# Performance work log

Hardware: AMD Instinct MI355X
Metric: run time of the kernel (lower is better)

## Reference

```python
import jax, jax.numpy as jnp
import numpy as np

B = 4096
D = 512
N_IMG = 8


def setup_inputs() -> dict:
    key = jax.random.key(0)
    k1, k2 = jax.random.split(key)
    feat_query = jax.random.normal(k1, (B, D), dtype=jnp.float32)
    feat_gallery = jax.random.normal(k2, (B, D), dtype=jnp.float32)
    return {"feat_query": feat_query, "feat_gallery": feat_gallery, "batch_size_image": N_IMG}


def _forward(feat_query, feat_gallery, batch_size_image):
    b = feat_query.shape[0]
    labels = jnp.arange(b) // batch_size_image
    pos_full = (labels[:, None] == labels[None, :]).astype(feat_query.dtype)  # [B,B] block-diag
    neg_mask = 1.0 - pos_full
    pos_dist_diag = pos_full * 1e25
    pos_mask = pos_full - jnp.eye(b, dtype=feat_query.dtype)  # positives excluding self

    # squared euclidean pairwise distance: ||q||^2 + ||g||^2 - 2 q.g
    nq = jnp.sum(feat_query * feat_query, axis=1, keepdims=True)          # [B,1]
    ng = jnp.sum(feat_gallery * feat_gallery, axis=1, keepdims=True)      # [B,1]
    r = feat_query @ feat_gallery.T                                        # [B,B] GEMM
    distance = jnp.clip(nq + ng.T - 2.0 * r, 1e-8, None)

    dist_pos = distance * pos_mask
    dist_neg = distance * neg_mask + pos_dist_diag

    # --- sampling on stop-gradient copies (mirrors .data usage in torch) ---
    dp = jax.lax.stop_gradient(dist_pos)
    dn = jax.lax.stop_gradient(dist_neg)
    skey = jax.random.key(42)
    kp, kn = jax.random.split(skey)

    # multinomial over positive distances == categorical with zero-weight elsewhere
    neg_inf = jnp.float32(-jnp.inf)
    logw_pos = jnp.where(dp > 0, jnp.log(dp), neg_inf)
    pos_ids = jax.random.categorical(kp, logw_pos, axis=-1)                # [B]
    pscore = jnp.take_along_axis(dp, pos_ids[:, None], axis=1)[:, 0]       # [B]

    # uniform among negatives with dist < pscore + 1e-4; fallback to argmin
    hard_mask = dn < (pscore[:, None] + 1e-4)                              # [B,B]
    logw_neg = jnp.where(hard_mask, 0.0, neg_inf)
    neg_sampled = jax.random.categorical(kn, logw_neg, axis=-1)            # [B]
    neg_ids = jnp.where(hard_mask.any(axis=-1), neg_sampled, jnp.argmin(dn, axis=-1))

    score_pos = jnp.sqrt(jnp.take_along_axis(dist_pos, pos_ids[:, None], axis=1))  # [B,1]
    score_neg = jnp.sqrt(jnp.take_along_axis(dist_neg, neg_ids[:, None], axis=1))  # [B,1]

    # margin == 0 branch: softplus loss
    diff = 1e-4 + score_pos - score_neg
    loss = jnp.mean(jax.nn.softplus(diff))
    return loss


def reference(feat_query, feat_gallery, batch_size_image):
    return _forward(feat_query, feat_gallery, batch_size_image)
```

## Files before the change

kernel.cpp:

```cpp
#include <hip/hip_runtime.h>
#include <hip/hip_fp16.h>
#include <stdint.h>
#include <math.h>

#define B 4096
#define D 512
#define NIMG_SHIFT 3

#define BM 128
#define BN 128
#define NKS 8
#define NCH (B / BN)

typedef _Float16 f16x8 __attribute__((ext_vector_type(8)));
typedef float f32x4 __attribute__((ext_vector_type(4)));

#define LDSPTR(p) ((__attribute__((address_space(3))) void*)(p))
#define GLPTR(p)  ((const __attribute__((address_space(1))) void*)(p))

__device__ __half   Q2h[(size_t)B * D];
__device__ __half   G2h[(size_t)B * D];
__device__ float    nqd[B], ngd[B], psd[B], spd[B];
__device__ uint32_t bKeyd[NCH * B];
__device__ float    bDnd[NCH * B];
__device__ float    mDnd[NCH * B];
__device__ float    partd[B / 8];

__host__ __device__ inline void tf2x32(uint32_t k0, uint32_t k1,
                                       uint32_t x0, uint32_t x1,
                                       uint32_t& y0, uint32_t& y1) {
  const uint32_t ks2 = k0 ^ k1 ^ 0x1BD11BDAu;
  uint32_t v0 = x0 + k0, v1 = x1 + k1;
#define RR(r) { v0 += v1; v1 = (v1 << (r)) | (v1 >> (32 - (r))); v1 ^= v0; }
  RR(13) RR(15) RR(26) RR(6)   v0 += k1;  v1 += ks2 + 1u;
  RR(17) RR(29) RR(16) RR(24)  v0 += ks2; v1 += k0 + 2u;
  RR(13) RR(15) RR(26) RR(6)   v0 += k0;  v1 += k1 + 3u;
  RR(17) RR(29) RR(16) RR(24)  v0 += k1;  v1 += ks2 + 4u;
  RR(13) RR(15) RR(26) RR(6)   v0 += ks2; v1 += k0 + 5u;
#undef RR
  y0 = v0; y1 = v1;
}

__device__ inline uint32_t draw_bits(uint32_t key0, uint32_t key1, uint32_t flat) {
  uint32_t y0, y1;
  tf2x32(key0, key1, 0u, flat, y0, y1);
  return y1;
}

__device__ inline float gumbel_from_bits(uint32_t bits) {
  float f = __uint_as_float((bits >> 9) | 0x3f800000u) - 1.0f;
  float u = (f == 0.0f) ? 1.17549435e-38f : f;
  return -logf(-logf(u));
}

__global__ __launch_bounds__(256) void cvtn_k(const float* __restrict__ Q,
                                              const float* __restrict__ G) {
  int gtid = blockIdx.x * 256 + threadIdx.x;
  int wave = gtid >> 6;
  int lane = gtid & 63;
  if (wave >= 2 * B) return;
  const int isG = wave >= B;
  const float* src = isG ? G : Q;
  __half* dst = isG ? G2h : Q2h;
  const int row = isG ? wave - B : wave;
  const float4* p = (const float4*)(src + (size_t)row * D);
  float ssq = 0.0f;
#pragma unroll
  for (int i = 0; i < 2; i++) {
    const int e = lane + 64 * i;
    float4 v = p[e];
    const float* pv = (const float*)&v;
    __half hh[4] __attribute__((aligned(8)));
#pragma unroll
    for (int j = 0; j < 4; j++) {
      const float x = pv[j];
      ssq += x * x;
      hh[j] = __float2half(x);
    }
    *(uint2*)(dst + (size_t)row * D + e * 4) = *(const uint2*)hh;
  }
#pragma unroll
  for (int off = 32; off; off >>= 1) ssq += __shfl_xor(ssq, off, 64);
  if (lane == 0) { if (isG) ngd[row] = ssq; else nqd[row] = ssq; }
}

__global__ __launch_bounds__(256) void pos_k(const float* __restrict__ Q,
                                             const float* __restrict__ G,
                                             uint32_t kp0, uint32_t kp1) {
  __shared__ float Qs[8][D];
  __shared__ float Gs[8][D];
  __shared__ float dots[8][8];
  int t = threadIdx.x;
  int rbase = blockIdx.x * 8;
#pragma unroll
  for (int s = 0; s < 4; s++) {
    int idx = t + 256 * s;
    int rr = idx >> 7;
    int kk = idx & 127;
    ((float4*)&Qs[rr][0])[kk] = ((const float4*)(Q + (size_t)(rbase + rr) * D))[kk];
    ((float4*)&Gs[rr][0])[kk] = ((const float4*)(G + (size_t)(rbase + rr) * D))[kk];
  }
  __syncthreads();
  {
    int p = t >> 2;
    int part = t & 3;
    int i = p >> 3, j = p & 7;
    float s = 0.0f;
    int k0 = part * 128;
    for (int k = k0; k < k0 + 128; k++) s += Qs[i][k] * Gs[j][k];
    s += __shfl_xor(s, 1, 64);
    s += __shfl_xor(s, 2, 64);
    if (part == 0) dots[i][j] = s;
  }
  __syncthreads();
  if (t < 8) {
    int i = t;
    int r = rbase + i;
    float nqr = nqd[r];
    float best = -INFINITY;
    float bdp = 0.0f;
#pragma unroll
    for (int j = 0; j < 8; j++) {
      if (j == i) continue;
      int c = rbase + j;
      float dp = fmaxf(nqr + ngd[c] - 2.0f * dots[i][j], 1e-8f);
      uint32_t bits = draw_bits(kp0, kp1, (uint32_t)(r * B + c));
      float logit = logf(dp) + gumbel_from_bits(bits);
      if (logit > best) { best = logit; bdp = dp; }
    }
    psd[r] = bdp;
    spd[r] = sqrtf(bdp);
  }
}

__global__ __launch_bounds__(512) void neg_k(uint32_t kn0, uint32_t kn1) {
  __shared__ char lds[65536] __attribute__((aligned(16)));
  const int t = threadIdx.x;
  const int l = t & 63;
  const int w = t >> 6;
  const int wr = w >> 1;
  const int wc = w & 1;
  const int lane16 = l & 15, g16 = l >> 4;
  const int r0 = blockIdx.y * BM;
  const int c0 = blockIdx.x * BN;

  f32x4 acc[2][4];
#pragma unroll
  for (int mi = 0; mi < 2; mi++)
#pragma unroll
    for (int nj = 0; nj < 4; nj++) acc[mi][nj] = (f32x4){0.f, 0.f, 0.f, 0.f};

  const char* qbase = (const char*)Q2h + (size_t)r0 * 1024;
  const char* gbase = (const char*)G2h + (size_t)c0 * 1024;

  int li[2], rc[2];
#pragma unroll
  for (int s = 0; s < 2; s++) {
    li[s] = t * 16 + s * 8192;
    const int aa = li[s] ^ (((li[s] >> 7) & 7) << 4);
    rc[s] = (aa >> 7) * 1024 + (aa & 127);
  }

  int offA[2], offA2[2], offB[4], offB2[4];
#pragma unroll
  for (int i = 0; i < 2; i++) {
    const int a = (wr * 32 + i * 16 + lane16) * 128 + g16 * 16;
    offA[i] = a ^ (((a >> 7) & 7) << 4);
    offA2[i] = offA[i] ^ 64;
  }
#pragma unroll
  for (int i = 0; i < 4; i++) {
    const int b = (wc * 64 + i * 16 + lane16) * 128 + g16 * 16;
    offB[i] = b ^ (((b >> 7) & 7) << 4);
    offB2[i] = offB[i] ^ 64;
  }

#define GLDS(SRC, DOFF) __builtin_amdgcn_global_load_lds(GLPTR(SRC), LDSPTR(lds + (DOFF)), 16, 0, 0)

#define STAGE(BUF, KS) do {                                            \
    _Pragma("unroll")                                                  \
    for (int s = 0; s < 2; s++) {                                      \
      GLDS(qbase + rc[s] + (KS) * 128, (BUF) * 32768 + li[s]);         \
      GLDS(gbase + rc[s] + (KS) * 128, (BUF) * 32768 + 16384 + li[s]); \
    }                                                                  \
  } while (0)

#define COMPUTE(BUF) do {                                                    \
    const char* lsrc = lds + (BUF) * 32768;                                  \
    f16x8 av[2][2], bv[4][2];                                                \
    _Pragma("unroll")                                                        \
    for (int i = 0; i < 2; i++) {                                            \
      av[i][0] = *(const f16x8*)(lsrc + offA[i]);                            \
      av[i][1] = *(const f16x8*)(lsrc + offA2[i]);                           \
    }                                                                        \
    _Pragma("unroll")                                                        \
    for (int i = 0; i < 4; i++) {                                            \
      bv[i][0] = *(const f16x8*)(lsrc + 16384 + offB[i]);                    \
      bv[i][1] = *(const f16x8*)(lsrc + 16384 + offB2[i]);                   \
    }                                                                        \
    _Pragma("unroll")                                                        \
    for (int kk = 0; kk < 2; kk++)                                           \
      _Pragma("unroll")                                                      \
      for (int nj = 0; nj < 4; nj++)                                         \
        _Pragma("unroll")                                                    \
        for (int mi = 0; mi < 2; mi++)                                       \
          acc[mi][nj] = __builtin_amdgcn_mfma_f32_16x16x32_f16(av[mi][kk], bv[nj][kk], acc[mi][nj], 0, 0, 0); \
  } while (0)

#define VM4  asm volatile("s_waitcnt vmcnt(4)" ::: "memory")
#define VM0  asm volatile("s_waitcnt vmcnt(0)" ::: "memory")
#define BAR  __builtin_amdgcn_s_barrier()

  STAGE(0, 0);
  STAGE(1, 1); VM4; BAR; COMPUTE(0); BAR;
  STAGE(0, 2); VM4; BAR; COMPUTE(1); BAR;
  STAGE(1, 3); VM4; BAR; COMPUTE(0); BAR;
  STAGE(0, 4); VM4; BAR; COMPUTE(1); BAR;
  STAGE(1, 5); VM4; BAR; COMPUTE(0); BAR;
  STAGE(0, 6); VM4; BAR; COMPUTE(1); BAR;
  STAGE(1, 7); VM4; BAR; COMPUTE(0); BAR;
               VM0; BAR; COMPUTE(1);
#undef STAGE
#undef COMPUTE
#undef GLDS
#undef VM4
#undef VM0
#undef BAR
  __syncthreads();

  uint32_t* pKey = (uint32_t*)lds;
  float*    pD   = (float*)(pKey + 256);
  float*    pM   = pD + 256;

  float ngv4[4];
  int cg4[4], cc4[4];
#pragma unroll
  for (int nj = 0; nj < 4; nj++) {
    const int c = c0 + wc * 64 + nj * 16 + lane16;
    ngv4[nj] = ngd[c];
    cg4[nj] = c >> NIMG_SHIFT;
    cc4[nj] = c;
  }

#pragma unroll
  for (int mi = 0; mi < 2; mi++) {
    const int rbase = r0 + wr * 32 + mi * 16 + g16 * 4;
    const float4 nq4 = *(const float4*)(nqd + rbase);
    const float4 ps4 = *(const float4*)(psd + rbase);
#pragma unroll
    for (int q = 0; q < 4; q++) {
      const int rr = wr * 32 + mi * 16 + g16 * 4 + q;
      const int rg = (rbase + q) >> NIMG_SHIFT;
      const float nqv = ((const float*)&nq4)[q];
      const float thr = ((const float*)&ps4)[q] + 1e-4f;
      uint32_t bKey = 0u, bC = 0xFFFFFFFFu, mC = 0xFFFFFFFFu;
      float bD = 0.0f, mD = INFINITY;
#pragma unroll
      for (int nj = 0; nj < 4; nj++) {
        const float dv = fmaxf(nqv + ngv4[nj] - 2.0f * acc[mi][nj][q], 1e-8f);
        const float dn = (cg4[nj] == rg) ? 1e25f : dv;
        if (dn < mD) { mD = dn; mC = (uint32_t)cc4[nj]; }
        if (dn < thr) {
          const uint32_t bits = draw_bits(kn0, kn1, (uint32_t)(((rbase + q) << 12) | cc4[nj]));
          const uint32_t key = (bits >> 9) + 1u;
          if (key > bKey) { bKey = key; bC = (uint32_t)cc4[nj]; bD = dn; }
        }
      }
#pragma unroll
      for (int off = 8; off >= 1; off >>= 1) {
        const uint32_t kO = __shfl_xor(bKey, off, 64);
        const uint32_t cO = __shfl_xor(bC, off, 64);
        const float dO = __shfl_xor(bD, off, 64);
        if (kO > bKey || (kO == bKey && cO < bC)) { bKey = kO; bC = cO; bD = dO; }
        const float mdO = __shfl_xor(mD, off, 64);
        const uint32_t mcO = __shfl_xor(mC, off, 64);
        if (mdO < mD || (mdO == mD && mcO < mC)) { mD = mdO; mC = mcO; }
      }
      if (lane16 == 0) {
        const int idx = wc * 128 + rr;
        pKey[idx] = bKey; pD[idx] = bD; pM[idx] = mD;
      }
    }
  }
  __syncthreads();
  if (t < 128) {
    const uint32_t k0 = pKey[t], k1 = pKey[t + 128];
    const float d0 = pD[t], d1 = pD[t + 128];
    const uint32_t bk = (k1 > k0) ? k1 : k0;
    const float bd = (k1 > k0) ? d1 : d0;
    const float m0 = pM[t], m1 = pM[t + 128];
    const float md = (m1 < m0) ? m1 : m0;
    const int p = blockIdx.x * B + (r0 + t);
    bKeyd[p] = bk; bDnd[p] = bd; mDnd[p] = md;
  }
}

__global__ __launch_bounds__(256) void fin1_k() {
  __shared__ float red[8];
  const int t = threadIdx.x;
  const int lrow = t >> 5;
  const int ch = t & 31;
  const int r = blockIdx.x * 8 + lrow;
  const int p = ch * B + r;
  uint32_t bk = bKeyd[p];
  uint32_t bch = (uint32_t)ch;
  float bd = bDnd[p];
  float md = mDnd[p];
  uint32_t mch = (uint32_t)ch;
#pragma unroll
  for (int off = 16; off >= 1; off >>= 1) {
    const uint32_t kO = __shfl_xor(bk, off, 64);
    const uint32_t cO = __shfl_xor(bch, off, 64);
    const float dO = __shfl_xor(bd, off, 64);
    if (kO > bk || (kO == bk && cO < bch)) { bk = kO; bch = cO; bd = dO; }
    const float mO = __shfl_xor(md, off, 64);
    const uint32_t mcO = __shfl_xor(mch, off, 64);
    if (mO < md || (mO == md && mcO < mch)) { md = mO; mch = mcO; }
  }
  if (ch == 0) {
    const float dn = (bk != 0u) ? bd : md;
    const float x = 1e-4f + spd[r] - sqrtf(dn);
    red[lrow] = fmaxf(x, 0.0f) + log1pf(expf(-fabsf(x)));
  }
  __syncthreads();
  if (t == 0) {
    float s = 0.0f;
#pragma unroll
    for (int i = 0; i < 8; i++) s += red[i];
    partd[blockIdx.x] = s;
  }
}

__global__ __launch_bounds__(256) void fin2_k(float* __restrict__ out) {
  __shared__ float red[256];
  const int t = threadIdx.x;
  red[t] = partd[t] + partd[t + 256];
  __syncthreads();
#pragma unroll
  for (int s = 128; s; s >>= 1) {
    if (t < s) red[t] += red[t + s];
    __syncthreads();
  }
  if (t == 0) out[0] = red[0] * (1.0f / (float)B);
}

extern "C" void kernel_launch(void* const* d_in, const int* in_sizes, int n_in,
                              void* d_out, int out_size, void* d_ws, size_t ws_size,
                              hipStream_t stream) {
  (void)in_sizes; (void)n_in; (void)out_size; (void)d_ws; (void)ws_size;
  const float* Q = (const float*)d_in[0];
  const float* G = (const float*)d_in[1];
  float* out = (float*)d_out;

  uint32_t kp0, kp1, kn0, kn1;
  tf2x32(0u, 42u, 0u, 0u, kp0, kp1);
  tf2x32(0u, 42u, 0u, 1u, kn0, kn1);

  hipLaunchKernelGGL(cvtn_k, dim3(2 * B / 4), dim3(256), 0, stream, Q, G);
  hipLaunchKernelGGL(pos_k, dim3(B / 8), dim3(256), 0, stream, Q, G, kp0, kp1);
  hipLaunchKernelGGL(neg_k, dim3(B / BN, B / BM), dim3(512), 0, stream, kn0, kn1);
  hipLaunchKernelGGL(fin1_k, dim3(B / 8), dim3(256), 0, stream);
  hipLaunchKernelGGL(fin2_k, dim3(1), dim3(256), 0, stream, out);
}
```

Baseline: 92.99 us.

## Fuse fp16 conversion into positive kernel and precompute RNG keys during GEMM

Merges the fp16 conversion and norm kernel into the positive-sampling kernel, so Q and G are read from global memory once and one launch is dropped. In the negative kernel, Threefry random keys for every element of the tile are computed unconditionally, interleaved with the async LDS load stages, so ALU work overlaps memory latency. The epilogue then selects precomputed keys instead of calling the RNG under a data-dependent branch. This adds 32 live registers per thread, which may lower occupancy, and computes keys even for elements that fail the threshold.

```diff
diff --git a/kernel.cpp b/kernel.cpp
--- a/kernel.cpp
+++ b/kernel.cpp
@@ -53,45 +53,15 @@
   return -logf(-logf(u));
 }
 
-__global__ __launch_bounds__(256) void cvtn_k(const float* __restrict__ Q,
-                                              const float* __restrict__ G) {
-  int gtid = blockIdx.x * 256 + threadIdx.x;
-  int wave = gtid >> 6;
-  int lane = gtid & 63;
-  if (wave >= 2 * B) return;
-  const int isG = wave >= B;
-  const float* src = isG ? G : Q;
-  __half* dst = isG ? G2h : Q2h;
-  const int row = isG ? wave - B : wave;
-  const float4* p = (const float4*)(src + (size_t)row * D);
-  float ssq = 0.0f;
-#pragma unroll
-  for (int i = 0; i < 2; i++) {
-    const int e = lane + 64 * i;
-    float4 v = p[e];
-    const float* pv = (const float*)&v;
-    __half hh[4] __attribute__((aligned(8)));
-#pragma unroll
-    for (int j = 0; j < 4; j++) {
-      const float x = pv[j];
-      ssq += x * x;
-      hh[j] = __float2half(x);
-    }
-    *(uint2*)(dst + (size_t)row * D + e * 4) = *(const uint2*)hh;
-  }
-#pragma unroll
-  for (int off = 32; off; off >>= 1) ssq += __shfl_xor(ssq, off, 64);
-  if (lane == 0) { if (isG) ngd[row] = ssq; else nqd[row] = ssq; }
-}
-
-__global__ __launch_bounds__(256) void pos_k(const float* __restrict__ Q,
+__global__ __launch_bounds__(256) void cvp_k(const float* __restrict__ Q,
                                              const float* __restrict__ G,
                                              uint32_t kp0, uint32_t kp1) {
   __shared__ float Qs[8][D];
   __shared__ float Gs[8][D];
   __shared__ float dots[8][8];
-  int t = threadIdx.x;
-  int rbase = blockIdx.x * 8;
+  __shared__ float nql[8], ngl[8];
+  const int t = threadIdx.x;
+  const int rbase = blockIdx.x * 8;
 #pragma unroll
   for (int s = 0; s < 4; s++) {
     int idx = t + 256 * s;
@@ -99,6 +69,43 @@
     int kk = idx & 127;
     ((float4*)&Qs[rr][0])[kk] = ((const float4*)(Q + (size_t)(rbase + rr) * D))[kk];
     ((float4*)&Gs[rr][0])[kk] = ((const float4*)(G + (size_t)(rbase + rr) * D))[kk];
+  }
+  __syncthreads();
+#pragma unroll
+  for (int s = 0; s < 4; s++) {
+    int idx = t + 256 * s;
+    int rr = idx >> 7;
+    int kk = idx & 127;
+    float4 vq = ((const float4*)&Qs[rr][0])[kk];
+    float4 vg = ((const float4*)&Gs[rr][0])[kk];
+    __half hq[4] __attribute__((aligned(8)));
+    __half hg[4] __attribute__((aligned(8)));
+    const float* pq = (const float*)&vq;
+    const float* pg = (const float*)&vg;
+#pragma unroll
+    for (int j = 0; j < 4; j++) { hq[j] = __float2half(pq[j]); hg[j] = __float2half(pg[j]); }
+    *(uint2*)(Q2h + (size_t)(rbase + rr) * D + kk * 4) = *(const uint2*)hq;
+    *(uint2*)(G2h + (size_t)(rbase + rr) * D + kk * 4) = *(const uint2*)hg;
+  }
+  {
+    const int wave = t >> 6, lane = t & 63;
+#pragma unroll
+    for (int rr2 = 0; rr2 < 4; rr2++) {
+      const int rowid = wave * 4 + rr2;
+      const float* src = (rowid < 8) ? &Qs[rowid][0] : &Gs[rowid - 8][0];
+      float ssq = 0.0f;
+#pragma unroll
+      for (int i = 0; i < 2; i++) {
+        float4 v = ((const float4*)src)[lane + 64 * i];
+        ssq += v.x * v.x + v.y * v.y + v.z * v.z + v.w * v.w;
+      }
+#pragma unroll
+      for (int off = 32; off; off >>= 1) ssq += __shfl_xor(ssq, off, 64);
+      if (lane == 0) {
+        if (rowid < 8) { nqd[rbase + rowid] = ssq; nql[rowid] = ssq; }
+        else           { ngd[rbase + rowid - 8] = ssq; ngl[rowid - 8] = ssq; }
+      }
+    }
   }
   __syncthreads();
   {
@@ -116,14 +123,14 @@
   if (t < 8) {
     int i = t;
     int r = rbase + i;
-    float nqr = nqd[r];
+    float nqr = nql[i];
     float best = -INFINITY;
     float bdp = 0.0f;
 #pragma unroll
     for (int j = 0; j < 8; j++) {
       if (j == i) continue;
       int c = rbase + j;
-      float dp = fmaxf(nqr + ngd[c] - 2.0f * dots[i][j], 1e-8f);
+      float dp = fmaxf(nqr + ngl[j] - 2.0f * dots[i][j], 1e-8f);
       uint32_t bits = draw_bits(kp0, kp1, (uint32_t)(r * B + c));
       float logit = logf(dp) + gumbel_from_bits(bits);
       if (logit > best) { best = logit; bdp = dp; }
@@ -174,6 +181,18 @@
     offB[i] = b ^ (((b >> 7) & 7) << 4);
     offB2[i] = offB[i] ^ 64;
   }
+
+  uint32_t keys[32];
+
+#define KEYS4(K) do {                                                          \
+    const int mi_ = (K) >> 2, q_ = (K) & 3;                                    \
+    const uint32_t rr_ = (uint32_t)(r0 + wr * 32 + mi_ * 16 + g16 * 4 + q_);   \
+    _Pragma("unroll")                                                          \
+    for (int nj = 0; nj < 4; nj++) {                                           \
+      const uint32_t cc_ = (uint32_t)(c0 + wc * 64 + nj * 16 + lane16);        \
+      keys[(K) * 4 + nj] = (draw_bits(kn0, kn1, (rr_ << 12) | cc_) >> 9) + 1u; \
+    }                                                                          \
+  } while (0)
 
 #define GLDS(SRC, DOFF) __builtin_amdgcn_global_load_lds(GLPTR(SRC), LDSPTR(lds + (DOFF)), 16, 0, 0)
 
@@ -211,14 +230,14 @@
 #define VM0  asm volatile("s_waitcnt vmcnt(0)" ::: "memory")
 #define BAR  __builtin_amdgcn_s_barrier()
 
-  STAGE(0, 0);
-  STAGE(1, 1); VM4; BAR; COMPUTE(0); BAR;
-  STAGE(0, 2); VM4; BAR; COMPUTE(1); BAR;
-  STAGE(1, 3); VM4; BAR; COMPUTE(0); BAR;
-  STAGE(0, 4); VM4; BAR; COMPUTE(1); BAR;
-  STAGE(1, 5); VM4; BAR; COMPUTE(0); BAR;
-  STAGE(0, 6); VM4; BAR; COMPUTE(1); BAR;
-  STAGE(1, 7); VM4; BAR; COMPUTE(0); BAR;
+  STAGE(0, 0); KEYS4(0);
+  STAGE(1, 1); KEYS4(1); VM4; BAR; COMPUTE(0); BAR;
+  STAGE(0, 2); KEYS4(2); VM4; BAR; COMPUTE(1); BAR;
+  STAGE(1, 3); KEYS4(3); VM4; BAR; COMPUTE(0); BAR;
+  STAGE(0, 4); KEYS4(4); VM4; BAR; COMPUTE(1); BAR;
+  STAGE(1, 5); KEYS4(5); VM4; BAR; COMPUTE(0); BAR;
+  STAGE(0, 6); KEYS4(6); VM4; BAR; COMPUTE(1); BAR;
+  STAGE(1, 7); KEYS4(7); VM4; BAR; COMPUTE(0); BAR;
                VM0; BAR; COMPUTE(1);
 #undef STAGE
 #undef COMPUTE
@@ -226,6 +245,7 @@
 #undef VM4
 #undef VM0
 #undef BAR
+#undef KEYS4
   __syncthreads();
 
   uint32_t* pKey = (uint32_t*)lds;
@@ -260,11 +280,8 @@
         const float dv = fmaxf(nqv + ngv4[nj] - 2.0f * acc[mi][nj][q], 1e-8f);
         const float dn = (cg4[nj] == rg) ? 1e25f : dv;
         if (dn < mD) { mD = dn; mC = (uint32_t)cc4[nj]; }
-        if (dn < thr) {
-          const uint32_t bits = draw_bits(kn0, kn1, (uint32_t)(((rbase + q) << 12) | cc4[nj]));
-          const uint32_t key = (bits >> 9) + 1u;
-          if (key > bKey) { bKey = key; bC = (uint32_t)cc4[nj]; bD = dn; }
-        }
+        const uint32_t key = (dn < thr) ? keys[mi * 16 + q * 4 + nj] : 0u;
+        if (key > bKey) { bKey = key; bC = (uint32_t)cc4[nj]; bD = dn; }
       }
 #pragma unroll
       for (int off = 8; off >= 1; off >>= 1) {
@@ -356,8 +373,7 @@
   tf2x32(0u, 42u, 0u, 0u, kp0, kp1);
   tf2x32(0u, 42u, 0u, 1u, kn0, kn1);
 
-  hipLaunchKernelGGL(cvtn_k, dim3(2 * B / 4), dim3(256), 0, stream, Q, G);
-  hipLaunchKernelGGL(pos_k, dim3(B / 8), dim3(256), 0, stream, Q, G, kp0, kp1);
+  hipLaunchKernelGGL(cvp_k, dim3(B / 8), dim3(256), 0, stream, Q, G, kp0, kp1);
   hipLaunchKernelGGL(neg_k, dim3(B / BN, B / BM), dim3(512), 0, stream, kn0, kn1);
   hipLaunchKernelGGL(fin1_k, dim3(B / 8), dim3(256), 0, stream);
   hipLaunchKernelGGL(fin2_k, dim3(1), dim3(256), 0, stream, out);
```

Measured after the change: 83.24 us, median of 3. 1.12x faster.
